# Performance work log

Measured on AMD Instinct MI355X. Metric: run time of the kernel, lower is better.

The kernel has to match this reference:

```python
import jax, jax.numpy as jnp
import numpy as np

N = 100000      # n_nodes
E = 1600000     # n_edges (avg degree 16)
IN, H, OUT = 128, 128, 64


def setup_inputs() -> dict:
    key = jax.random.key(0)
    ks = jax.random.split(key, 10)
    x = jax.random.normal(ks[0], (N, IN), dtype=jnp.float32)
    edge_index = jax.random.randint(ks[1], (2, E), 0, N, dtype=jnp.int32)
    def glorot(k, fan_in, fan_out):
        return jax.random.normal(k, (fan_in, fan_out), dtype=jnp.float32) * (1.0 / np.sqrt(fan_in))
    W0 = glorot(ks[2], IN, H)
    b0 = jnp.zeros((H,), jnp.float32)
    W1 = glorot(ks[3], H, H)
    b1 = jnp.zeros((H,), jnp.float32)
    W2 = glorot(ks[4], H, OUT)
    b2 = jnp.zeros((OUT,), jnp.float32)
    Ws = glorot(ks[5], H, H)            # skip_connections[0]
    bs = jax.random.normal(ks[6], (H,), jnp.float32) * 0.01
    return {"x": x, "edge_index": edge_index, "W0": W0, "b0": b0,
            "W1": W1, "b1": b1, "W2": W2, "b2": b2, "Ws": Ws, "bs": bs}


def _gcn_conv(h, W, b, src, dst, deg_isqrt):
    # GCNConv: out = D^-1/2 (A+I) D^-1/2 (h @ W) + b
    hw = h @ W                                   # [N, F_out]
    norm = deg_isqrt[src] * deg_isqrt[dst]       # [E+N]
    msg = hw[src] * norm[:, None]                # gather + scale
    return jax.ops.segment_sum(msg, dst, num_segments=N) + b


def reference(x, edge_index, W0, b0, W1, b1, W2, b2, Ws, bs):
    loops = jnp.arange(N, dtype=edge_index.dtype)
    src = jnp.concatenate([edge_index[0], loops])   # self-loops appended
    dst = jnp.concatenate([edge_index[1], loops])
    deg = jax.ops.segment_sum(jnp.ones_like(dst, jnp.float32), dst, num_segments=N)
    deg_isqrt = jnp.where(deg > 0, jax.lax.rsqrt(jnp.maximum(deg, 1e-12)), 0.0)

    # layer 0 (dropout = identity in eval mode)
    h = jax.nn.relu(_gcn_conv(x, W0, b0, src, dst, deg_isqrt))
    # layer 1 with residual skip Linear
    identity = h
    h = jax.nn.relu(_gcn_conv(h, W1, b1, src, dst, deg_isqrt))
    h = h + identity @ Ws + bs
    # output layer
    return _gcn_conv(h, W2, b2, src, dst, deg_isqrt)
```

## Files before the change

### kernel.cpp

```cpp
#include <hip/hip_runtime.h>

#define ELLW 64
#define BSHIFT 9
#define BNODES 512
#define NBUCK  256
#define BCAP   12288

typedef __attribute__((ext_vector_type(8))) short short8v;
typedef __attribute__((ext_vector_type(4))) float f32x4;

__device__ inline unsigned short bf16_rne(float x) {
    unsigned u = __float_as_uint(x);
    u += 0x7FFFu + ((u >> 16) & 1u);
    return (unsigned short)(u >> 16);
}
__device__ inline float bf16_to_f32(unsigned short h) {
    return __uint_as_float(((unsigned)h) << 16);
}

__global__ __launch_bounds__(256) void partition_kernel(
    const int* __restrict__ src, const int* __restrict__ dst, int E,
    uint2* __restrict__ part, int* __restrict__ gtail)
{
    __shared__ int scnt[NBUCK];
    __shared__ int sbase[NBUCK];
    const int t = threadIdx.x;
    #pragma unroll
    for (int i = t; i < NBUCK; i += 256) scnt[i] = 0;
    __syncthreads();

    const int e0 = blockIdx.x * 2048;
    int sarr[8], darr[8], rk[8];
    #pragma unroll
    for (int i = 0; i < 8; ++i) {
        int e = e0 + t + i * 256;
        if (e < E) {
            sarr[i] = src[e];
            darr[i] = dst[e];
            rk[i] = atomicAdd(&scnt[darr[i] >> BSHIFT], 1);
        }
    }
    __syncthreads();
    for (int i = t; i < NBUCK; i += 256)
        sbase[i] = scnt[i] ? atomicAdd(&gtail[i], scnt[i]) : 0;
    __syncthreads();
    #pragma unroll
    for (int i = 0; i < 8; ++i) {
        int e = e0 + t + i * 256;
        if (e < E) {
            int b = darr[i] >> BSHIFT;
            int p = sbase[b] + rk[i];
            if (p < BCAP)
                part[(size_t)b * BCAP + p] = make_uint2((unsigned)sarr[i], (unsigned)darr[i]);
        }
    }
}

__global__ __launch_bounds__(512) void ell_bucket_kernel(
    const uint2* __restrict__ part, const int* __restrict__ gcnt,
    int* __restrict__ degi, float* __restrict__ dinv,
    int* __restrict__ ell, int n)
{
    __shared__ int sdeg[BNODES];
    __shared__ int sell[BNODES * ELLW];

    const int b = blockIdx.x;
    const int t = threadIdx.x;
    sdeg[t] = 0;
    __syncthreads();

    int cnt = gcnt[b];
    if (cnt > BCAP) cnt = BCAP;
    const uint2* ep = part + (size_t)b * BCAP;
    for (int i = t; i < cnt; i += 512) {
        uint2 e = ep[i];
        int dl = (int)(e.y & (BNODES - 1));
        int pos = atomicAdd(&sdeg[dl], 1);
        if (pos < ELLW) sell[dl * ELLW + pos] = (int)e.x;
    }
    __syncthreads();

    const int node0 = b << BSHIFT;
    const int node = node0 + t;
    if (node < n) {
        int d = sdeg[t];
        degi[node] = d;
        dinv[node] = rsqrtf((float)d + 1.0f);
    }
    for (int f4 = t; f4 < BNODES * ELLW / 4; f4 += 512) {
        int nd = node0 + (f4 >> 4);
        if (nd < n) {
            int4 v = *(const int4*)&sell[f4 * 4];
            *(int4*)&ell[(size_t)node0 * ELLW + f4 * 4] = v;
        }
    }
}

__global__ __launch_bounds__(256) void split_all_w_kernel(
    const float* __restrict__ W0, const float* __restrict__ W1,
    const float* __restrict__ Ws, const float* __restrict__ W2,
    unsigned short* __restrict__ W0hi, unsigned short* __restrict__ W0lo,
    unsigned short* __restrict__ W1hi, unsigned short* __restrict__ W1lo,
    unsigned short* __restrict__ Wshi, unsigned short* __restrict__ Wslo,
    unsigned short* __restrict__ W2hi, unsigned short* __restrict__ W2lo)
{
    int id = blockIdx.x * 256 + threadIdx.x;
    const float* W; unsigned short *Whi, *Wlo; int F, base;
    if (id < 16384)      { W = W0; Whi = W0hi; Wlo = W0lo; F = 128; base = 0; }
    else if (id < 32768) { W = W1; Whi = W1hi; Wlo = W1lo; F = 128; base = 16384; }
    else if (id < 49152) { W = Ws; Whi = Wshi; Wlo = Wslo; F = 128; base = 32768; }
    else if (id < 57344) { W = W2; Whi = W2hi; Wlo = W2lo; F = 64;  base = 49152; }
    else return;
    int l = id - base;
    int k = l / F, c = l % F;
    float x = W[l];
    unsigned short hi = bf16_rne(x);
    Whi[c * 128 + k] = hi;
    Wlo[c * 128 + k] = bf16_rne(x - bf16_to_f32(hi));
}

template<int F, bool AFP32, bool BIAS>
__global__ __launch_bounds__(256) void mfma_gemm_kernel(
    const float* __restrict__ Af,
    const unsigned short* __restrict__ Ahi, const unsigned short* __restrict__ Alo,
    const unsigned short* __restrict__ BhiT, const unsigned short* __restrict__ BloT,
    const float* __restrict__ bias, unsigned short* __restrict__ out, int nrows)
{
    constexpr int WM = (F == 128) ? 2 : 4;
    constexpr int MF = 128 / (WM * 16);
    constexpr int CG = 4;

    const int t    = threadIdx.x;
    const int lane = t & 63;
    const int wv   = t >> 6;
    const int wm   = (F == 128) ? (wv >> 1) : wv;
    const int wn   = (F == 128) ? (wv & 1)  : 0;
    const int l15  = lane & 15;
    const int lg   = lane >> 4;
    const int row0 = blockIdx.x * 128;

    f32x4 acc[MF][CG];
    #pragma unroll
    for (int mf = 0; mf < MF; ++mf)
        #pragma unroll
        for (int cg = 0; cg < CG; ++cg)
            acc[mf][cg] = (f32x4){0.f, 0.f, 0.f, 0.f};

    #pragma unroll
    for (int kk = 0; kk < 4; ++kk) {
        short8v ah[MF], al[MF];
        #pragma unroll
        for (int mf = 0; mf < MF; ++mf) {
            int row = row0 + wm * (MF * 16) + mf * 16 + l15;
            int rl  = row < nrows ? row : 0;
            size_t ao = (size_t)rl * 128 + kk * 32 + lg * 8;
            if constexpr (AFP32) {
                const float* p = &Af[ao];
                float4 v0 = *(const float4*)p;
                float4 v1 = *(const float4*)(p + 4);
                float xs[8] = {v0.x, v0.y, v0.z, v0.w, v1.x, v1.y, v1.z, v1.w};
                short8v h, l;
                #pragma unroll
                for (int j = 0; j < 8; ++j) {
                    unsigned short hb = bf16_rne(xs[j]);
                    h[j] = (short)hb;
                    l[j] = (short)bf16_rne(xs[j] - bf16_to_f32(hb));
                }
                ah[mf] = h; al[mf] = l;
            } else {
                ah[mf] = *(const short8v*)&Ahi[ao];
                al[mf] = *(const short8v*)&Alo[ao];
            }
        }
        #pragma unroll
        for (int cg = 0; cg < CG; ++cg) {
            int col = wn * 64 + cg * 16 + l15;
            size_t bo = (size_t)col * 128 + kk * 32 + lg * 8;
            short8v bh = *(const short8v*)&BhiT[bo];
            short8v bl = *(const short8v*)&BloT[bo];
            #pragma unroll
            for (int mf = 0; mf < MF; ++mf) {
                acc[mf][cg] = __builtin_amdgcn_mfma_f32_16x16x32_bf16(ah[mf], bh, acc[mf][cg], 0, 0, 0);
                acc[mf][cg] = __builtin_amdgcn_mfma_f32_16x16x32_bf16(ah[mf], bl, acc[mf][cg], 0, 0, 0);
                acc[mf][cg] = __builtin_amdgcn_mfma_f32_16x16x32_bf16(al[mf], bh, acc[mf][cg], 0, 0, 0);
            }
        }
    }

    #pragma unroll
    for (int cg = 0; cg < CG; ++cg) {
        int col = wn * 64 + cg * 16 + l15;
        float bv = BIAS ? bias[col] : 0.f;
        #pragma unroll
        for (int mf = 0; mf < MF; ++mf) {
            int rbase = row0 + wm * (MF * 16) + mf * 16 + lg * 4;
            #pragma unroll
            for (int r = 0; r < 4; ++r) {
                int row = rbase + r;
                if (row < nrows)
                    out[(size_t)row * F + col] = bf16_rne(acc[mf][cg][r] + bv);
            }
        }
    }
}

template<int F, int MODE>
__global__ __launch_bounds__(256) void agg_kernel(
    const unsigned short* __restrict__ hw, const int* __restrict__ ell,
    const int* __restrict__ degi, const float* __restrict__ dinv,
    const float* __restrict__ bias, const unsigned short* __restrict__ skip,
    unsigned* __restrict__ outHi, unsigned* __restrict__ outLo,
    float* __restrict__ outF, int n)
{
    constexpr int VEC = F / 64;
    constexpr int UNR = 8;
    const int lane = threadIdx.x & 63;
    const int node = blockIdx.x * 4 + (threadIdx.x >> 6);
    if (node >= n) return;

    const int deg  = degi[node];
    const int kmax = deg < ELLW ? deg : ELLW;
    const float di = dinv[node];

    int   jpre = 0;
    float vpre = 0.f;
    if (lane < kmax) {
        jpre = ell[node * ELLW + lane];
        vpre = dinv[jpre];
    }

    float acc[4][VEC];
    #pragma unroll
    for (int u = 0; u < 4; ++u)
        #pragma unroll
        for (int v = 0; v < VEC; ++v) acc[u][v] = 0.f;

    if constexpr (VEC == 2) {
        unsigned p = *(const unsigned*)&hw[(size_t)node * F + lane * 2];
        acc[0][0] = bf16_to_f32((unsigned short)(p & 0xFFFF)) * di;
        acc[0][1] = bf16_to_f32((unsigned short)(p >> 16)) * di;
    } else {
        acc[0][0] = bf16_to_f32(hw[(size_t)node * F + lane]) * di;
    }

    const int kceil = (kmax + UNR - 1) & ~(UNR - 1);
    for (int k = 0; k < kceil; k += UNR) {
        int   jj[UNR];
        float vv[UNR];
        #pragma unroll
        for (int u = 0; u < UNR; ++u) {
            jj[u] = __shfl(jpre, k + u);
            vv[u] = __shfl(vpre, k + u);
        }
        if constexpr (VEC == 2) {
            unsigned h[UNR];
            #pragma unroll
            for (int u = 0; u < UNR; ++u)
                h[u] = *(const unsigned*)&hw[(size_t)jj[u] * F + lane * 2];
            #pragma unroll
            for (int u = 0; u < UNR; ++u) {
                acc[u & 3][0] += bf16_to_f32((unsigned short)(h[u] & 0xFFFF)) * vv[u];
                acc[u & 3][1] += bf16_to_f32((unsigned short)(h[u] >> 16)) * vv[u];
            }
        } else {
            unsigned short h[UNR];
            #pragma unroll
            for (int u = 0; u < UNR; ++u)
                h[u] = hw[(size_t)jj[u] * F + lane];
            #pragma unroll
            for (int u = 0; u < UNR; ++u)
                acc[u & 3][0] += bf16_to_f32(h[u]) * vv[u];
        }
    }

    float r[VEC];
    #pragma unroll
    for (int v = 0; v < VEC; ++v) {
        float s = (acc[0][v] + acc[1][v]) + (acc[2][v] + acc[3][v]);
        r[v] = s * di + bias[lane * VEC + v];
    }

    if constexpr (MODE == 2) {
        outF[(size_t)node * F + lane] = r[0];
    } else {
        #pragma unroll
        for (int v = 0; v < VEC; ++v) {
            r[v] = fmaxf(r[v], 0.f);
            if (MODE == 1) {
                unsigned sp = *(const unsigned*)&skip[(size_t)node * F + lane * 2];
                float sv = (v == 0) ? bf16_to_f32((unsigned short)(sp & 0xFFFF))
                                    : bf16_to_f32((unsigned short)(sp >> 16));
                r[v] += sv;
            }
        }
        unsigned short h0 = bf16_rne(r[0]), h1 = bf16_rne(r[1]);
        unsigned short l0 = bf16_rne(r[0] - bf16_to_f32(h0));
        unsigned short l1 = bf16_rne(r[1] - bf16_to_f32(h1));
        size_t o = (size_t)node * (F / 2) + lane;
        outHi[o] = (unsigned)h0 | ((unsigned)h1 << 16);
        outLo[o] = (unsigned)l0 | ((unsigned)l1 << 16);
    }
}

extern "C" void kernel_launch(void* const* d_in, const int* in_sizes, int n_in,
                              void* d_out, int out_size, void* d_ws, size_t ws_size,
                              hipStream_t stream)
{
    const float* x  = (const float*)d_in[0];
    const int*   ei = (const int*)  d_in[1];
    const float* W0 = (const float*)d_in[2];
    const float* b0 = (const float*)d_in[3];
    const float* W1 = (const float*)d_in[4];
    const float* b1 = (const float*)d_in[5];
    const float* W2 = (const float*)d_in[6];
    const float* b2 = (const float*)d_in[7];
    const float* Ws = (const float*)d_in[8];
    const float* bs = (const float*)d_in[9];

    const int N = in_sizes[0] / 128;
    const int E = in_sizes[1] / 2;
    const int* src = ei;
    const int* dst = ei + E;

    char* ws = (char*)d_ws;
    auto al = [](size_t v) { return (v + 255) & ~size_t(255); };
    size_t off = 0;
    int*   degi  = (int*)  (ws + off); off = al(off + (size_t)N * 4);
    float* dinv  = (float*)(ws + off); off = al(off + (size_t)N * 4);
    int*   gtail = (int*)  (ws + off); off = al(off + NBUCK * 4);
    int*   ell   = (int*)  (ws + off); off = al(off + (size_t)N * ELLW * 4);
    uint2* part  = (uint2*)(ws + off); off = al(off + (size_t)NBUCK * BCAP * 8);
    unsigned short* pA   = (unsigned short*)(ws + off); off = al(off + (size_t)N * 128 * 2);
    unsigned short* pBhi = (unsigned short*)(ws + off); off = al(off + (size_t)N * 128 * 2);
    unsigned short* pBlo = (unsigned short*)(ws + off); off = al(off + (size_t)N * 128 * 2);
    unsigned short* pC   = (unsigned short*)(ws + off); off = al(off + (size_t)N * 128 * 2);
    unsigned short* W0hi = (unsigned short*)(ws + off); off = al(off + 128 * 128 * 2);
    unsigned short* W0lo = (unsigned short*)(ws + off); off = al(off + 128 * 128 * 2);
    unsigned short* W1hi = (unsigned short*)(ws + off); off = al(off + 128 * 128 * 2);
    unsigned short* W1lo = (unsigned short*)(ws + off); off = al(off + 128 * 128 * 2);
    unsigned short* Wshi = (unsigned short*)(ws + off); off = al(off + 128 * 128 * 2);
    unsigned short* Wslo = (unsigned short*)(ws + off); off = al(off + 128 * 128 * 2);
    unsigned short* W2hi = (unsigned short*)(ws + off); off = al(off + 128 * 64 * 2);
    unsigned short* W2lo = (unsigned short*)(ws + off); off = al(off + 128 * 64 * 2);
    (void)ws_size; (void)n_in; (void)out_size;

    hipMemsetAsync(gtail, 0, NBUCK * 4, stream);
    partition_kernel<<<(E + 2047) / 2048, 256, 0, stream>>>(src, dst, E, part, gtail);
    ell_bucket_kernel<<<(N + BNODES - 1) / BNODES, 512, 0, stream>>>(
        part, gtail, degi, dinv, ell, N);
    split_all_w_kernel<<<224, 256, 0, stream>>>(
        W0, W1, Ws, W2, W0hi, W0lo, W1hi, W1lo, Wshi, Wslo, W2hi, W2lo);

    const int gg = (N + 127) / 128;
    const int ga = (N + 3) / 4;

    mfma_gemm_kernel<128, true, false><<<gg, 256, 0, stream>>>(
        x, nullptr, nullptr, W0hi, W0lo, nullptr, pA, N);
    agg_kernel<128, 0><<<ga, 256, 0, stream>>>(
        pA, ell, degi, dinv, b0, nullptr, (unsigned*)pBhi, (unsigned*)pBlo, nullptr, N);

    mfma_gemm_kernel<128, false, true><<<gg, 256, 0, stream>>>(
        nullptr, pBhi, pBlo, Wshi, Wslo, bs, pC, N);
    mfma_gemm_kernel<128, false, false><<<gg, 256, 0, stream>>>(
        nullptr, pBhi, pBlo, W1hi, W1lo, nullptr, pA, N);
    agg_kernel<128, 1><<<ga, 256, 0, stream>>>(
        pA, ell, degi, dinv, b1, pC, (unsigned*)pBhi, (unsigned*)pBlo, nullptr, N);

    mfma_gemm_kernel<64, false, false><<<gg, 256, 0, stream>>>(
        nullptr, pBhi, pBlo, W2hi, W2lo, nullptr, pA, N);
    agg_kernel<64, 2><<<ga, 256, 0, stream>>>(
        pA, ell, degi, dinv, b2, nullptr, nullptr, nullptr, (float*)d_out, N);
}
```

Before: 372.7 us.

## Prescale GEMM outputs by source dinv and fuse skip and W1 GEMMs

The GEMM epilogues now multiply each row by dinv, so aggregation no longer gathers dinv per neighbor or multiplies per edge. The skip-Linear and W1 GEMMs are merged into one 512-thread kernel that reads the shared A tile once and writes both outputs. Padded ELL lanes now point at a zeroed dummy row instead of being masked by a zero weight, which needs an extra memset and a padded buffer. For the F=64 layer the dummy index is 2N, which lands on zeroed padding only because of how the row stride works out, so it is fragile.

```diff
diff --git a/kernel.cpp b/kernel.cpp
--- a/kernel.cpp
+++ b/kernel.cpp
@@ -119,39 +119,34 @@
     Wlo[c * 128 + k] = bf16_rne(x - bf16_to_f32(hi));
 }
 
-template<int F, bool AFP32, bool BIAS>
-__global__ __launch_bounds__(256) void mfma_gemm_kernel(
+template<int F, bool AFP32>
+__global__ __launch_bounds__(256) void mfma_gemm_scaled_kernel(
     const float* __restrict__ Af,
     const unsigned short* __restrict__ Ahi, const unsigned short* __restrict__ Alo,
     const unsigned short* __restrict__ BhiT, const unsigned short* __restrict__ BloT,
-    const float* __restrict__ bias, unsigned short* __restrict__ out, int nrows)
-{
-    constexpr int WM = (F == 128) ? 2 : 4;
-    constexpr int MF = 128 / (WM * 16);
-    constexpr int CG = 4;
-
+    const float* __restrict__ dinv, unsigned short* __restrict__ out, int nrows)
+{
+    constexpr int CG = F / 16;
     const int t    = threadIdx.x;
     const int lane = t & 63;
     const int wv   = t >> 6;
-    const int wm   = (F == 128) ? (wv >> 1) : wv;
-    const int wn   = (F == 128) ? (wv & 1)  : 0;
     const int l15  = lane & 15;
     const int lg   = lane >> 4;
-    const int row0 = blockIdx.x * 128;
-
-    f32x4 acc[MF][CG];
-    #pragma unroll
-    for (int mf = 0; mf < MF; ++mf)
+    const int row0 = blockIdx.x * 128 + wv * 32;
+
+    f32x4 acc[2][CG];
+    #pragma unroll
+    for (int mf = 0; mf < 2; ++mf)
         #pragma unroll
         for (int cg = 0; cg < CG; ++cg)
             acc[mf][cg] = (f32x4){0.f, 0.f, 0.f, 0.f};
 
     #pragma unroll
     for (int kk = 0; kk < 4; ++kk) {
-        short8v ah[MF], al[MF];
-        #pragma unroll
-        for (int mf = 0; mf < MF; ++mf) {
-            int row = row0 + wm * (MF * 16) + mf * 16 + l15;
+        short8v ah[2], al[2];
+        #pragma unroll
+        for (int mf = 0; mf < 2; ++mf) {
+            int row = row0 + mf * 16 + l15;
             int rl  = row < nrows ? row : 0;
             size_t ao = (size_t)rl * 128 + kk * 32 + lg * 8;
             if constexpr (AFP32) {
@@ -174,12 +169,12 @@
         }
         #pragma unroll
         for (int cg = 0; cg < CG; ++cg) {
-            int col = wn * 64 + cg * 16 + l15;
+            int col = cg * 16 + l15;
             size_t bo = (size_t)col * 128 + kk * 32 + lg * 8;
             short8v bh = *(const short8v*)&BhiT[bo];
             short8v bl = *(const short8v*)&BloT[bo];
             #pragma unroll
-            for (int mf = 0; mf < MF; ++mf) {
+            for (int mf = 0; mf < 2; ++mf) {
                 acc[mf][cg] = __builtin_amdgcn_mfma_f32_16x16x32_bf16(ah[mf], bh, acc[mf][cg], 0, 0, 0);
                 acc[mf][cg] = __builtin_amdgcn_mfma_f32_16x16x32_bf16(ah[mf], bl, acc[mf][cg], 0, 0, 0);
                 acc[mf][cg] = __builtin_amdgcn_mfma_f32_16x16x32_bf16(al[mf], bh, acc[mf][cg], 0, 0, 0);
@@ -188,17 +183,102 @@
     }
 
     #pragma unroll
-    for (int cg = 0; cg < CG; ++cg) {
-        int col = wn * 64 + cg * 16 + l15;
-        float bv = BIAS ? bias[col] : 0.f;
-        #pragma unroll
-        for (int mf = 0; mf < MF; ++mf) {
-            int rbase = row0 + wm * (MF * 16) + mf * 16 + lg * 4;
+    for (int mf = 0; mf < 2; ++mf) {
+        int rbase = row0 + mf * 16 + lg * 4;
+        float dv[4];
+        #pragma unroll
+        for (int r = 0; r < 4; ++r)
+            dv[r] = (rbase + r < nrows) ? dinv[rbase + r] : 0.f;
+        #pragma unroll
+        for (int cg = 0; cg < CG; ++cg) {
+            int col = cg * 16 + l15;
             #pragma unroll
             for (int r = 0; r < 4; ++r) {
                 int row = rbase + r;
                 if (row < nrows)
-                    out[(size_t)row * F + col] = bf16_rne(acc[mf][cg][r] + bv);
+                    out[(size_t)row * F + col] = bf16_rne(acc[mf][cg][r] * dv[r]);
+            }
+        }
+    }
+}
+
+__global__ __launch_bounds__(512) void mfma_gemm_dual_kernel(
+    const unsigned short* __restrict__ Ahi, const unsigned short* __restrict__ Alo,
+    const unsigned short* __restrict__ WsHiT, const unsigned short* __restrict__ WsLoT,
+    const unsigned short* __restrict__ W1HiT, const unsigned short* __restrict__ W1LoT,
+    const float* __restrict__ bias_s, const float* __restrict__ dinv,
+    unsigned short* __restrict__ outS, unsigned short* __restrict__ outM, int nrows)
+{
+    const int t    = threadIdx.x;
+    const int lane = t & 63;
+    const int wv   = t >> 6;
+    const int wm   = wv >> 1;
+    const int wn   = wv & 1;
+    const int l15  = lane & 15;
+    const int lg   = lane >> 4;
+    const int row0 = blockIdx.x * 128 + wm * 32;
+
+    f32x4 accS[2][4], accM[2][4];
+    #pragma unroll
+    for (int mf = 0; mf < 2; ++mf)
+        #pragma unroll
+        for (int cg = 0; cg < 4; ++cg) {
+            accS[mf][cg] = (f32x4){0.f, 0.f, 0.f, 0.f};
+            accM[mf][cg] = (f32x4){0.f, 0.f, 0.f, 0.f};
+        }
+
+    #pragma unroll
+    for (int kk = 0; kk < 4; ++kk) {
+        short8v ah[2], al[2];
+        #pragma unroll
+        for (int mf = 0; mf < 2; ++mf) {
+            int row = row0 + mf * 16 + l15;
+            int rl  = row < nrows ? row : 0;
+            size_t ao = (size_t)rl * 128 + kk * 32 + lg * 8;
+            ah[mf] = *(const short8v*)&Ahi[ao];
+            al[mf] = *(const short8v*)&Alo[ao];
+        }
+        #pragma unroll
+        for (int cg = 0; cg < 4; ++cg) {
+            int col = wn * 64 + cg * 16 + l15;
+            size_t bo = (size_t)col * 128 + kk * 32 + lg * 8;
+            short8v sh = *(const short8v*)&WsHiT[bo];
+            short8v sl = *(const short8v*)&WsLoT[bo];
+            #pragma unroll
+            for (int mf = 0; mf < 2; ++mf) {
+                accS[mf][cg] = __builtin_amdgcn_mfma_f32_16x16x32_bf16(ah[mf], sh, accS[mf][cg], 0, 0, 0);
+                accS[mf][cg] = __builtin_amdgcn_mfma_f32_16x16x32_bf16(ah[mf], sl, accS[mf][cg], 0, 0, 0);
+                accS[mf][cg] = __builtin_amdgcn_mfma_f32_16x16x32_bf16(al[mf], sh, accS[mf][cg], 0, 0, 0);
+            }
+            short8v oh = *(const short8v*)&W1HiT[bo];
+            short8v ol = *(const short8v*)&W1LoT[bo];
+            #pragma unroll
+            for (int mf = 0; mf < 2; ++mf) {
+                accM[mf][cg] = __builtin_amdgcn_mfma_f32_16x16x32_bf16(ah[mf], oh, accM[mf][cg], 0, 0, 0);
+                accM[mf][cg] = __builtin_amdgcn_mfma_f32_16x16x32_bf16(ah[mf], ol, accM[mf][cg], 0, 0, 0);
+                accM[mf][cg] = __builtin_amdgcn_mfma_f32_16x16x32_bf16(al[mf], oh, accM[mf][cg], 0, 0, 0);
+            }
+        }
+    }
+
+    #pragma unroll
+    for (int mf = 0; mf < 2; ++mf) {
+        int rbase = row0 + mf * 16 + lg * 4;
+        float dv[4];
+        #pragma unroll
+        for (int r = 0; r < 4; ++r)
+            dv[r] = (rbase + r < nrows) ? dinv[rbase + r] : 0.f;
+        #pragma unroll
+        for (int cg = 0; cg < 4; ++cg) {
+            int col = wn * 64 + cg * 16 + l15;
+            float bv = bias_s[col];
+            #pragma unroll
+            for (int r = 0; r < 4; ++r) {
+                int row = rbase + r;
+                if (row < nrows) {
+                    outS[(size_t)row * 128 + col] = bf16_rne(accS[mf][cg][r] + bv);
+                    outM[(size_t)row * 128 + col] = bf16_rne(accM[mf][cg][r] * dv[r]);
+                }
             }
         }
     }
@@ -206,11 +286,11 @@
 
 template<int F, int MODE>
 __global__ __launch_bounds__(256) void agg_kernel(
-    const unsigned short* __restrict__ hw, const int* __restrict__ ell,
+    const unsigned short* __restrict__ hws, const int* __restrict__ ell,
     const int* __restrict__ degi, const float* __restrict__ dinv,
     const float* __restrict__ bias, const unsigned short* __restrict__ skip,
     unsigned* __restrict__ outHi, unsigned* __restrict__ outLo,
-    float* __restrict__ outF, int n)
+    float* __restrict__ outF, int n, int dummy)
 {
     constexpr int VEC = F / 64;
     constexpr int UNR = 8;
@@ -222,12 +302,8 @@
     const int kmax = deg < ELLW ? deg : ELLW;
     const float di = dinv[node];
 
-    int   jpre = 0;
-    float vpre = 0.f;
-    if (lane < kmax) {
-        jpre = ell[node * ELLW + lane];
-        vpre = dinv[jpre];
-    }
+    int jpre = dummy;
+    if (lane < kmax) jpre = ell[node * ELLW + lane];
 
     float acc[4][VEC];
     #pragma unroll
@@ -236,40 +312,36 @@
         for (int v = 0; v < VEC; ++v) acc[u][v] = 0.f;
 
     if constexpr (VEC == 2) {
-        unsigned p = *(const unsigned*)&hw[(size_t)node * F + lane * 2];
-        acc[0][0] = bf16_to_f32((unsigned short)(p & 0xFFFF)) * di;
-        acc[0][1] = bf16_to_f32((unsigned short)(p >> 16)) * di;
+        unsigned p = *(const unsigned*)&hws[(size_t)node * F + lane * 2];
+        acc[0][0] = bf16_to_f32((unsigned short)(p & 0xFFFF));
+        acc[0][1] = bf16_to_f32((unsigned short)(p >> 16));
     } else {
-        acc[0][0] = bf16_to_f32(hw[(size_t)node * F + lane]) * di;
+        acc[0][0] = bf16_to_f32(hws[(size_t)node * F + lane]);
     }
 
     const int kceil = (kmax + UNR - 1) & ~(UNR - 1);
     for (int k = 0; k < kceil; k += UNR) {
-        int   jj[UNR];
-        float vv[UNR];
-        #pragma unroll
-        for (int u = 0; u < UNR; ++u) {
-            jj[u] = __shfl(jpre, k + u);
-            vv[u] = __shfl(vpre, k + u);
-        }
+        int jj[UNR];
+        #pragma unroll
+        for (int u = 0; u < UNR; ++u) jj[u] = __shfl(jpre, k + u);
         if constexpr (VEC == 2) {
             unsigned h[UNR];
             #pragma unroll
             for (int u = 0; u < UNR; ++u)
-                h[u] = *(const unsigned*)&hw[(size_t)jj[u] * F + lane * 2];
+                h[u] = *(const unsigned*)&hws[(size_t)jj[u] * F + lane * 2];
             #pragma unroll
             for (int u = 0; u < UNR; ++u) {
-                acc[u & 3][0] += bf16_to_f32((unsigned short)(h[u] & 0xFFFF)) * vv[u];
-                acc[u & 3][1] += bf16_to_f32((unsigned short)(h[u] >> 16)) * vv[u];
+                acc[u & 3][0] += bf16_to_f32((unsigned short)(h[u] & 0xFFFF));
+                acc[u & 3][1] += bf16_to_f32((unsigned short)(h[u] >> 16));
             }
         } else {
             unsigned short h[UNR];
             #pragma unroll
             for (int u = 0; u < UNR; ++u)
-                h[u] = hw[(size_t)jj[u] * F + lane];
+                h[u] = hws[(size_t)jj[u] * F + lane];
             #pragma unroll
             for (int u = 0; u < UNR; ++u)
-                acc[u & 3][0] += bf16_to_f32(h[u]) * vv[u];
+                acc[u & 3][0] += bf16_to_f32(h[u]);
         }
     }
 
@@ -330,7 +402,7 @@
     int*   gtail = (int*)  (ws + off); off = al(off + NBUCK * 4);
     int*   ell   = (int*)  (ws + off); off = al(off + (size_t)N * ELLW * 4);
     uint2* part  = (uint2*)(ws + off); off = al(off + (size_t)NBUCK * BCAP * 8);
-    unsigned short* pA   = (unsigned short*)(ws + off); off = al(off + (size_t)N * 128 * 2);
+    unsigned short* pA   = (unsigned short*)(ws + off); off = al(off + ((size_t)N * 128 + 128) * 2);
     unsigned short* pBhi = (unsigned short*)(ws + off); off = al(off + (size_t)N * 128 * 2);
     unsigned short* pBlo = (unsigned short*)(ws + off); off = al(off + (size_t)N * 128 * 2);
     unsigned short* pC   = (unsigned short*)(ws + off); off = al(off + (size_t)N * 128 * 2);
@@ -345,6 +417,7 @@
     (void)ws_size; (void)n_in; (void)out_size;
 
     hipMemsetAsync(gtail, 0, NBUCK * 4, stream);
+    hipMemsetAsync(pA + (size_t)N * 128, 0, 128 * 2, stream);
     partition_kernel<<<(E + 2047) / 2048, 256, 0, stream>>>(src, dst, E, part, gtail);
     ell_bucket_kernel<<<(N + BNODES - 1) / BNODES, 512, 0, stream>>>(
         part, gtail, degi, dinv, ell, N);
@@ -354,20 +427,18 @@
     const int gg = (N + 127) / 128;
     const int ga = (N + 3) / 4;
 
-    mfma_gemm_kernel<128, true, false><<<gg, 256, 0, stream>>>(
-        x, nullptr, nullptr, W0hi, W0lo, nullptr, pA, N);
+    mfma_gemm_scaled_kernel<128, true><<<gg, 256, 0, stream>>>(
+        x, nullptr, nullptr, W0hi, W0lo, dinv, pA, N);
     agg_kernel<128, 0><<<ga, 256, 0, stream>>>(
-        pA, ell, degi, dinv, b0, nullptr, (unsigned*)pBhi, (unsigned*)pBlo, nullptr, N);
-
-    mfma_gemm_kernel<128, false, true><<<gg, 256, 0, stream>>>(
-        nullptr, pBhi, pBlo, Wshi, Wslo, bs, pC, N);
-    mfma_gemm_kernel<128, false, false><<<gg, 256, 0, stream>>>(
-        nullptr, pBhi, pBlo, W1hi, W1lo, nullptr, pA, N);
+        pA, ell, degi, dinv, b0, nullptr, (unsigned*)pBhi, (unsigned*)pBlo, nullptr, N, N);
+
+    mfma_gemm_dual_kernel<<<gg, 512, 0, stream>>>(
+        pBhi, pBlo, Wshi, Wslo, W1hi, W1lo, bs, dinv, pC, pA, N);
     agg_kernel<128, 1><<<ga, 256, 0, stream>>>(
-        pA, ell, degi, dinv, b1, pC, (unsigned*)pBhi, (unsigned*)pBlo, nullptr, N);
-
-    mfma_gemm_kernel<64, false, false><<<gg, 256, 0, stream>>>(
-        nullptr, pBhi, pBlo, W2hi, W2lo, nullptr, pA, N);
+        pA, ell, degi, dinv, b1, pC, (unsigned*)pBhi, (unsigned*)pBlo, nullptr, N, N);
+
+    mfma_gemm_scaled_kernel<64, false><<<gg, 256, 0, stream>>>(
+        nullptr, pBhi, pBlo, W2hi, W2lo, dinv, pA, N);
     agg_kernel<64, 2><<<ga, 256, 0, stream>>>(
-        pA, ell, degi, dinv, b2, nullptr, nullptr, nullptr, (float*)d_out, N);
-}
+        pA, ell, degi, dinv, b2, nullptr, nullptr, nullptr, (float*)d_out, N, 2 * N);
+}
```

Measured after the change: 395.0 us. +6.0%, slower.
